# Kernel optimization log

Hardware: AMD Instinct MI355X
Metric: run time of the kernel (lower is better)

## Reference

```python
import jax, jax.numpy as jnp
import numpy as np

# config (from UnifiedAttentionConfig defaults)
D = 512; H = 8; C = 64; DQ = 256; NI = 2; CI = 64
TOPK = 32; LMAX = 16; NWIN = 128; ROPE_BASE = 10000.0
B = 1; T = 1024; LP = 8; P = T // LP
NEG = -1e30


def _rope_cache(seq_len, dim):
    half = dim // 2
    inv = 1.0 / (ROPE_BASE ** (jnp.arange(half, dtype=jnp.float32) / half))
    f = jnp.arange(seq_len, dtype=jnp.float32)[:, None] * inv[None, :]
    emb = jnp.concatenate([f, f], axis=-1)
    return jnp.cos(emb), jnp.sin(emb)


def _rot(x, cos, sin):
    half = x.shape[-1] // 2
    x1, x2 = x[..., :half], x[..., half:]
    return x * cos + jnp.concatenate([-x2, x1], axis=-1) * sin


def _rms(x, w, eps=1e-6):
    return x * jax.lax.rsqrt(jnp.mean(x * x, axis=-1, keepdims=True) + eps) * w


def _forward(h, W_dq, W_uq, W_csa_kv, W_csa_z, B_csa, W_idx_kv, W_idx_z, B_idx,
             W_iuq, W_w, W_swkv, qnorm_w, knorm_w, W_o, sink_logits,
             phrase_mask, phrase_token_idx, phrase_end_pos):
    Bq, Tq, Dq = h.shape
    Pn, Lmax = phrase_mask.shape[1], phrase_mask.shape[2]
    scale = 1.0 / jnp.sqrt(jnp.float32(C))
    cos, sin = _rope_cache(Tq, C)
    cos_i, sin_i = _rope_cache(Tq, CI)
    # ---- queries: compress -> up-project -> RMSNorm -> RoPE (per-token) ----
    q_lat = h @ W_dq                                      # (B,T,DQ)
    q = (q_lat @ W_uq).reshape(Bq, Tq, H, C)
    q = _rot(_rms(q, qnorm_w), cos[:, None, :], sin[:, None, :])
    # ---- gather phrase tokens ----
    idx = phrase_token_idx.reshape(Bq, Pn * Lmax)
    hp = jnp.take_along_axis(h, idx[:, :, None], axis=1).reshape(Bq, Pn, Lmax, Dq)
    m = phrase_mask                                       # (B,P,Lmax) bool
    # ---- multi-head phrase compression (CSA KV) ----
    c_tok = (hp @ W_csa_kv).reshape(Bq, Pn, Lmax, H, C)
    z = (hp @ W_csa_z).reshape(Bq, Pn, Lmax, H, C) + B_csa[None, None]
    z = jnp.where(m[..., None, None], z, NEG)
    g = jax.nn.softmax(z, axis=2)
    g = jnp.where(m.any(axis=2)[:, :, None, None, None], g, 0.0)
    c_csa = jnp.sum(g * c_tok, axis=2)                    # (B,P,H,C) values
    pos = jnp.clip(phrase_end_pos, 0, Tq - 1)
    k_csa = _rot(_rms(c_csa, knorm_w), cos[pos][:, :, None, :], sin[pos][:, :, None, :])
    # ---- single-head phrase compression (indexer keys) ----
    ck = hp @ W_idx_kv                                    # (B,P,Lmax,CI)
    zk = hp @ W_idx_z + B_idx[None, None]
    zk = jnp.where(m[..., None], zk, NEG)
    gk = jax.nn.softmax(zk, axis=2)
    gk = jnp.where(m.any(axis=2)[:, :, None, None], gk, 0.0)
    k_idx = jnp.sum(gk * ck, axis=2)                      # (B,P,CI)
    k_idx = _rot(k_idx, cos_i[pos], sin_i[pos])
    # ---- lightning indexer + causal top-k routing ----
    q_i = (q_lat @ W_iuq).reshape(Bq, Tq, NI, CI)
    s = jax.nn.relu(jnp.einsum('bthd,bpd->bthp', q_i, k_idx))
    I = jnp.sum(s * (h @ W_w)[..., None], axis=2)         # (B,T,P)
    t_idx = jnp.arange(Tq)
    valid = (phrase_end_pos[:, None, :] <= t_idx[None, :, None]) & (phrase_end_pos[:, None, :] >= 0)
    I = jnp.where(valid, I, NEG)
    vals, sel = jax.lax.top_k(I, TOPK)                    # (B,T,K)
    sel_ok = vals > NEG * 0.5
    k_sel = jnp.take_along_axis(k_csa[:, None], sel[:, :, :, None, None], axis=2)  # (B,T,K,H,C)
    v_sel = jnp.take_along_axis(c_csa[:, None], sel[:, :, :, None, None], axis=2)
    logit_csa = jnp.einsum('bthc,btkhc->bthk', q, k_sel) * scale
    logit_csa = jnp.where(sel_ok[:, :, None, :], logit_csa, NEG)
    # ---- sliding window (fixed mode) ----
    kv = (h @ W_swkv).reshape(Bq, Tq, H, C)
    k_sw = _rot(_rms(kv, knorm_w), cos[:, None, :], sin[:, None, :])
    widx = t_idx[:, None] + jnp.arange(NWIN)[None, :] - (NWIN - 1)  # (T,W)
    w_ok = widx >= 0
    widx_c = jnp.clip(widx, 0, Tq - 1)
    k_win = k_sw[:, widx_c]                               # (B,T,W,H,C)
    v_win = kv[:, widx_c]
    logit_sw = jnp.einsum('bthc,btwhc->bthw', q, k_win) * scale
    logit_sw = jnp.where(w_ok[None, :, None, :], logit_sw, NEG)
    # ---- single softmax over [csa | window | sink] ----
    sink = jnp.broadcast_to(sink_logits.reshape(1, 1, H, 1), (Bq, Tq, H, 1))
    pattn = jax.nn.softmax(jnp.concatenate([logit_csa, logit_sw, sink], axis=-1), axis=-1)
    out = jnp.einsum('bthk,btkhc->bthc', pattn[..., :TOPK], v_sel) \
        + jnp.einsum('bthw,btwhc->bthc', pattn[..., TOPK:TOPK + NWIN], v_win)
    return out.reshape(Bq, Tq, H * C) @ W_o


def setup_inputs() -> dict:
    key = jax.random.key(0)
    ks = jax.random.split(key, 16)
    nrm = lambda k, shp: 0.02 * jax.random.normal(k, shp, dtype=jnp.float32)
    # structured phrases: phrase p covers tokens [p*LP, p*LP+LP), padded to LMAX
    l = np.arange(LMAX)
    mask = np.broadcast_to(l < LP, (B, P, LMAX)).copy()
    tok = np.minimum(l, LP - 1)[None, :] + (np.arange(P) * LP)[:, None]
    tok = np.broadcast_to(tok, (B, P, LMAX)).copy()
    end = np.broadcast_to(np.arange(P) * LP + LP - 1, (B, P)).copy()
    pid = np.broadcast_to(np.arange(T) // LP, (B, T)).copy()
    return {
        'h': jax.random.normal(ks[0], (B, T, D), dtype=jnp.float32),
        'phrase_mask': jnp.asarray(mask, dtype=bool),
        'phrase_token_idx': jnp.asarray(tok, dtype=jnp.int32),
        'phrase_end_pos': jnp.asarray(end, dtype=jnp.int32),
        'phrase_id': jnp.asarray(pid, dtype=jnp.int32),
        'W_dq': nrm(ks[1], (D, DQ)),
        'W_uq': nrm(ks[2], (DQ, H * C)),
        'W_csa_kv': nrm(ks[3], (D, H * C)),
        'W_csa_z': nrm(ks[4], (D, H * C)),
        'B_csa': nrm(ks[5], (LMAX, H, C)),
        'W_idx_kv': nrm(ks[6], (D, CI)),
        'W_idx_z': nrm(ks[7], (D, CI)),
        'B_idx': nrm(ks[8], (LMAX, CI)),
        'W_iuq': nrm(ks[9], (DQ, NI * CI)),
        'W_w': nrm(ks[10], (D, NI)),
        'W_swkv': nrm(ks[11], (D, H * C)),
        'qnorm_w': jnp.ones((C,), dtype=jnp.float32),
        'knorm_w': jnp.ones((C,), dtype=jnp.float32),
        'W_o': nrm(ks[12], (H * C, D)),
        'sink_logits': nrm(ks[13], (H,)),
    }


def reference(h, phrase_mask, phrase_token_idx, phrase_end_pos, phrase_id,
              W_dq, W_uq, W_csa_kv, W_csa_z, B_csa, W_idx_kv, W_idx_z, B_idx,
              W_iuq, W_w, W_swkv, qnorm_w, knorm_w, W_o, sink_logits):
    del phrase_id  # only used when sw_mode == 'phrase'
    return _forward(h, W_dq, W_uq, W_csa_kv, W_csa_z, B_csa, W_idx_kv, W_idx_z,
                    B_idx, W_iuq, W_w, W_swkv, qnorm_w, knorm_w, W_o, sink_logits,
                    phrase_mask, phrase_token_idx, phrase_end_pos)
```

## Files before the change

kernel.cpp:

```cpp
#include <hip/hip_runtime.h>
#include <cmath>

static constexpr int Tn = 1024, Dn = 512, Hn = 8, Cn = 64, DQn = 256,
                     NIn = 2, CIn = 64, TK = 32, LM = 16, NW = 128, Pn = 128;
#define NEGV (-1e30f)

typedef unsigned short u16;
typedef __bf16 bf16x8 __attribute__((ext_vector_type(8)));
typedef float f32x4 __attribute__((ext_vector_type(4)));

__device__ __forceinline__ u16 f2bf(float x) {
  unsigned u = __float_as_uint(x);
  return (u16)((u + 0x7fffu + ((u >> 16) & 1u)) >> 16);
}
__device__ __forceinline__ float bf2f(u16 b) {
  return __uint_as_float((unsigned)b << 16);
}

struct PackJobs {
  const float* src[7];
  u16* dst[7];
  int start[8];
  int N[7];
  int logN[7];
  int isA[7];
  int ps[7];
};

__global__ __launch_bounds__(256) void pack_all(PackJobs pj) {
  int i = blockIdx.x * 256 + threadIdx.x;
  if (i >= pj.start[7]) return;
  int j = 0;
  while (i >= pj.start[j + 1]) ++j;
  int local = i - pj.start[j];
  const float* s = pj.src[j];
  u16* dh = pj.dst[j];
  u16* dl = dh + pj.ps[j];
  float x[8];
  size_t idx;
  if (pj.isA[j]) {
    int m = local & 1023;
    int kg = local >> 10;
    const float4* p = reinterpret_cast<const float4*>(s + (size_t)m * 512 + kg * 8);
    float4 a = p[0], b = p[1];
    x[0] = a.x; x[1] = a.y; x[2] = a.z; x[3] = a.w;
    x[4] = b.x; x[5] = b.y; x[6] = b.z; x[7] = b.w;
    idx = ((size_t)kg * 1024 + m) * 8;
  } else {
    int N = pj.N[j];
    int n = local & (N - 1);
    int kg = local >> pj.logN[j];
#pragma unroll
    for (int e = 0; e < 8; ++e) x[e] = s[(size_t)(kg * 8 + e) * N + n];
    idx = ((size_t)kg * N + n) * 8;
  }
  union { u16 u[8]; int4 v; } oh, ol;
#pragma unroll
  for (int e = 0; e < 8; ++e) {
    u16 hb = f2bf(x[e]);
    oh.u[e] = hb;
    ol.u[e] = f2bf(x[e] - bf2f(hb));
  }
  *reinterpret_cast<int4*>(dh + idx) = oh.v;
  *reinterpret_cast<int4*>(dl + idx) = ol.v;
}

struct TileDesc {
  const u16* Blo;
  const u16* Bhi;
  float* Clo;
  float* Chi;
  u16* Cp;
  int ldNlo, ldNhi, ldClo, ldChi, mode, n0, bps, cpps;
};
struct GemmArgs {
  TileDesc d[15];
};

#define GLD16(gp, lp)                                                     \
  __builtin_amdgcn_global_load_lds(                                      \
      (const __attribute__((address_space(1))) unsigned int*)(gp),       \
      (__attribute__((address_space(3))) unsigned int*)(lp), 16, 0, 0)

template <int FMW>
__global__ __launch_bounds__(256) void gemm_bf16(const u16* __restrict__ Ap,
                                                 int NK, int aps, GemmArgs ga) {
  constexpr int MT = FMW * 32;
  const int ct = blockIdx.x, rt = blockIdx.y;
  const TileDesc d = ga.d[ct];
  const int m0 = rt * MT;
  __shared__ __align__(16) u16 lA[2][2][4][MT][8];
  __shared__ __align__(16) u16 lB[2][2][4][128][8];
  const int tid = threadIdx.x;
  const int w = tid >> 6, lane = tid & 63;
  const int wm = w >> 1, wn = w & 1;

  f32x4 acc[FMW][4];
#pragma unroll
  for (int a = 0; a < FMW; ++a)
#pragma unroll
    for (int b = 0; b < 4; ++b)
#pragma unroll
      for (int r = 0; r < 4; ++r) acc[a][b][r] = 0.f;

  auto stage = [&](int buf, int kg) {
#pragma unroll
    for (int r0 = 0; r0 < MT; r0 += 64) {
      GLD16(Ap + ((size_t)kg * 1024 + m0 + r0 + lane) * 8, &lA[buf][0][w][r0][0]);
      GLD16(Ap + aps + ((size_t)kg * 1024 + m0 + r0 + lane) * 8, &lA[buf][1][w][r0][0]);
    }
    GLD16(d.Blo + ((size_t)kg * d.ldNlo + lane) * 8, &lB[buf][0][w][0][0]);
    GLD16(d.Bhi + ((size_t)kg * d.ldNhi + lane) * 8, &lB[buf][0][w][64][0]);
    GLD16(d.Blo + d.bps + ((size_t)kg * d.ldNlo + lane) * 8, &lB[buf][1][w][0][0]);
    GLD16(d.Bhi + d.bps + ((size_t)kg * d.ldNhi + lane) * 8, &lB[buf][1][w][64][0]);
  };

  stage(0, w);
  const int kq = lane >> 4, fr = lane & 15;
  for (int ks = 0; ks < NK; ++ks) {
    __syncthreads();
    if (ks + 1 < NK) stage((ks + 1) & 1, (ks + 1) * 4 + w);
    const int cb = ks & 1;
    bf16x8 aFh[FMW], aFl[FMW], bFh[4], bFl[4];
#pragma unroll
    for (int f = 0; f < FMW; ++f) {
      aFh[f] = *reinterpret_cast<const bf16x8*>(&lA[cb][0][kq][wm * (FMW * 16) + f * 16 + fr][0]);
      aFl[f] = *reinterpret_cast<const bf16x8*>(&lA[cb][1][kq][wm * (FMW * 16) + f * 16 + fr][0]);
    }
#pragma unroll
    for (int f = 0; f < 4; ++f) {
      bFh[f] = *reinterpret_cast<const bf16x8*>(&lB[cb][0][kq][wn * 64 + f * 16 + fr][0]);
      bFl[f] = *reinterpret_cast<const bf16x8*>(&lB[cb][1][kq][wn * 64 + f * 16 + fr][0]);
    }
#pragma unroll
    for (int fm = 0; fm < FMW; ++fm)
#pragma unroll
      for (int fn = 0; fn < 4; ++fn) {
        acc[fm][fn] = __builtin_amdgcn_mfma_f32_16x16x32_bf16(aFh[fm], bFh[fn],
                                                              acc[fm][fn], 0, 0, 0);
        acc[fm][fn] = __builtin_amdgcn_mfma_f32_16x16x32_bf16(aFl[fm], bFh[fn],
                                                              acc[fm][fn], 0, 0, 0);
        acc[fm][fn] = __builtin_amdgcn_mfma_f32_16x16x32_bf16(aFh[fm], bFl[fn],
                                                              acc[fm][fn], 0, 0, 0);
      }
  }
  float* Cb = (wn == 0) ? d.Clo : d.Chi;
  const int ldc = (wn == 0) ? d.ldClo : d.ldChi;
  if (d.mode != 1) {
#pragma unroll
    for (int fm = 0; fm < FMW; ++fm)
#pragma unroll
      for (int fn = 0; fn < 4; ++fn)
#pragma unroll
        for (int r = 0; r < 4; ++r) {
          int row = m0 + wm * (FMW * 16) + fm * 16 + (lane >> 4) * 4 + r;
          int cl = fn * 16 + fr;
          Cb[(size_t)row * ldc + cl] = acc[fm][fn][r];
        }
  }
  if (d.mode >= 1) {
#pragma unroll
    for (int fm = 0; fm < FMW; ++fm)
#pragma unroll
      for (int fn = 0; fn < 4; ++fn)
#pragma unroll
        for (int r = 0; r < 4; ++r) {
          int row = m0 + wm * (FMW * 16) + fm * 16 + (lane >> 4) * 4 + r;
          int gc = d.n0 + wn * 64 + fn * 16 + fr;
          float v = acc[fm][fn][r];
          u16 hb = f2bf(v);
          u16 lb = f2bf(v - bf2f(hb));
          size_t idx = ((size_t)(gc >> 3) * 1024 + row) * 8 + (gc & 7);
          d.Cp[idx] = hb;
          d.Cp[idx + d.cpps] = lb;
        }
  }
}

__global__ __launch_bounds__(256) void idx_kernel(
    const float* __restrict__ h, const float* __restrict__ q_lat,
    const float* __restrict__ Wikv, const float* __restrict__ Wiz,
    const float* __restrict__ Wiuq, float* __restrict__ hikv,
    float* __restrict__ hiz, float* __restrict__ qib) {
  const int t0 = blockIdx.x * 4;
  const int tid = threadIdx.x;
  __shared__ float hs[4][Dn];
  __shared__ float ql[4][DQn];
  for (int i = tid; i < 4 * Dn; i += 256)
    hs[i >> 9][i & 511] = h[(size_t)(t0 + (i >> 9)) * Dn + (i & 511)];
  for (int i = tid; i < 4 * DQn; i += 256)
    ql[i >> 8][i & 255] = q_lat[(size_t)(t0 + (i >> 8)) * DQn + (i & 255)];
  __syncthreads();
  if (tid < 128) {
    const float* Wm = (tid < 64) ? Wikv : Wiz;
    const int ci = tid & 63;
    float a0 = 0.f, a1 = 0.f, a2 = 0.f, a3 = 0.f;
#pragma unroll 8
    for (int k = 0; k < Dn; ++k) {
      float wv = Wm[k * CIn + ci];
      a0 += hs[0][k] * wv;
      a1 += hs[1][k] * wv;
      a2 += hs[2][k] * wv;
      a3 += hs[3][k] * wv;
    }
    float* dst = (tid < 64) ? hikv : hiz;
    dst[(size_t)(t0 + 0) * CIn + ci] = a0;
    dst[(size_t)(t0 + 1) * CIn + ci] = a1;
    dst[(size_t)(t0 + 2) * CIn + ci] = a2;
    dst[(size_t)(t0 + 3) * CIn + ci] = a3;
  } else {
    const int jj = tid - 128;
    float a0 = 0.f, a1 = 0.f, a2 = 0.f, a3 = 0.f;
#pragma unroll 8
    for (int k = 0; k < DQn; ++k) {
      float wv = Wiuq[k * 128 + jj];
      a0 += ql[0][k] * wv;
      a1 += ql[1][k] * wv;
      a2 += ql[2][k] * wv;
      a3 += ql[3][k] * wv;
    }
    qib[(size_t)(t0 + 0) * 128 + jj] = a0;
    qib[(size_t)(t0 + 1) * 128 + jj] = a1;
    qib[(size_t)(t0 + 2) * 128 + jj] = a2;
    qib[(size_t)(t0 + 3) * 128 + jj] = a3;
  }
}

__global__ __launch_bounds__(512) void phrase_rope_kernel(
    const int* __restrict__ maskbuf, const int* __restrict__ tokbuf,
    const int* __restrict__ endbuf, const float* __restrict__ hckv,
    const float* __restrict__ hcz, const float* __restrict__ hikv,
    const float* __restrict__ hiz, const float* __restrict__ Bcsa,
    const float* __restrict__ Bidx, const float* __restrict__ knw,
    const float* __restrict__ qnw, float* __restrict__ ccsa,
    float* __restrict__ kcsa, float* __restrict__ kidx,
    float* __restrict__ q, const float* __restrict__ kv,
    float* __restrict__ ksw) {
  const int tid = threadIdx.x;
  const int c = tid & 63;
  const float sgn = (c < 32) ? -1.f : 1.f;

  if (blockIdx.x >= Pn) {
    const int t = blockIdx.x - Pn;
    const float fr = (float)t * powf(10000.0f, -(float)(c & 31) / 32.0f);
    const float cv = cosf(fr), sv = sinf(fr);
    {
      float x = q[t * Dn + tid];
      float ss = x * x;
#pragma unroll
      for (int off = 32; off; off >>= 1) ss += __shfl_xor(ss, off, 64);
      float xr = x * rsqrtf(ss / (float)Cn + 1e-6f) * qnw[c];
      float pr = __shfl_xor(xr, 32, 64);
      q[t * Dn + tid] = xr * cv + sgn * pr * sv;
    }
    {
      float y = kv[t * Dn + tid];
      float ss = y * y;
#pragma unroll
      for (int off = 32; off; off >>= 1) ss += __shfl_xor(ss, off, 64);
      float yr = y * rsqrtf(ss / (float)Cn + 1e-6f) * knw[c];
      float pr = __shfl_xor(yr, 32, 64);
      ksw[t * Dn + tid] = yr * cv + sgn * pr * sv;
    }
    return;
  }

  const int p = blockIdx.x;
  __shared__ int s_bytemode;
  __shared__ int s_tok[LM];
  __shared__ int s_m[LM];
  __shared__ int s_pos, s_anyv;

  if (tid == 0) s_bytemode = 0;
  __syncthreads();
  {
    unsigned wv = ((const unsigned*)maskbuf)[tid];
    if (wv > 1u) atomicOr(&s_bytemode, 1);
  }
  __syncthreads();
  const int bytemode = s_bytemode;
  if (tid < LM) {
    int mv;
    if (bytemode)
      mv = ((const unsigned char*)maskbuf)[p * LM + tid] != 0;
    else
      mv = maskbuf[p * LM + tid] != 0;
    s_m[tid] = mv;
    s_tok[tid] = tokbuf[p * LM + tid];
  }
  if (tid == 0) {
    int e = endbuf[p];
    s_pos = min(max(e, 0), Tn - 1);
  }
  __syncthreads();
  if (tid == 0) {
    int any = 0;
    for (int l = 0; l < LM; ++l) any |= s_m[l];
    s_anyv = any;
  }
  __syncthreads();
  const int anyv = s_anyv;
  const int pos = s_pos;
  const float fr = (float)pos * powf(10000.0f, -(float)(c & 31) / 32.0f);
  const float cv = cosf(fr), sv = sinf(fr);

  {
    float z[LM];
    float zmax = NEGV;
#pragma unroll
    for (int l = 0; l < LM; ++l) {
      float zv = hcz[s_tok[l] * Dn + tid] + Bcsa[l * (Hn * Cn) + tid];
      zv = s_m[l] ? zv : NEGV;
      z[l] = zv;
      zmax = fmaxf(zmax, zv);
    }
    float den = 0.f, num = 0.f;
#pragma unroll
    for (int l = 0; l < LM; ++l) {
      float e = expf(z[l] - zmax);
      den += e;
      num += e * hckv[s_tok[l] * Dn + tid];
    }
    float cc = anyv ? (num / den) : 0.f;
    ccsa[p * (Hn * Cn) + tid] = cc;

    float ss = cc * cc;
#pragma unroll
    for (int off = 32; off; off >>= 1) ss += __shfl_xor(ss, off, 64);
    float kn = cc * rsqrtf(ss / (float)Cn + 1e-6f) * knw[c];
    float pr = __shfl_xor(kn, 32, 64);
    kcsa[p * (Hn * Cn) + tid] = kn * cv + sgn * pr * sv;
  }

  if (tid < CIn) {
    float zk[LM];
    float zm = NEGV;
#pragma unroll
    for (int l = 0; l < LM; ++l) {
      float zv = hiz[s_tok[l] * CIn + tid] + Bidx[l * CIn + tid];
      zv = s_m[l] ? zv : NEGV;
      zk[l] = zv;
      zm = fmaxf(zm, zv);
    }
    float dk = 0.f, nk = 0.f;
#pragma unroll
    for (int l = 0; l < LM; ++l) {
      float e = expf(zk[l] - zm);
      dk += e;
      nk += e * hikv[s_tok[l] * CIn + tid];
    }
    float ki = anyv ? (nk / dk) : 0.f;
    float pr = __shfl_xor(ki, 32, 64);
    kidx[p * CIn + tid] = ki * cv + sgn * pr * sv;
  }
}

__global__ __launch_bounds__(128) void score_topk_kernel(
    const float* __restrict__ hbuf, const float* __restrict__ Ww,
    const float* __restrict__ qi, const float* __restrict__ kidx,
    const int* __restrict__ endbuf, int* __restrict__ sel,
    int* __restrict__ selok) {
  const int t = blockIdx.x;
  const int tid = threadIdx.x;
  __shared__ float sqi[NIn * CIn];
  __shared__ float kT[CIn][Pn + 1];
  __shared__ float sI[Pn];
  __shared__ float sp0[128], sp1[128];

  sqi[tid] = qi[(size_t)t * (NIn * CIn) + tid];
#pragma unroll
  for (int it = 0; it < 16; ++it) {
    int idx4 = it * 128 + tid;
    float4 v = reinterpret_cast<const float4*>(kidx)[idx4];
    int p = idx4 >> 4;
    int c4 = (idx4 & 15) * 4;
    kT[c4 + 0][p] = v.x;
    kT[c4 + 1][p] = v.y;
    kT[c4 + 2][p] = v.z;
    kT[c4 + 3][p] = v.w;
  }
  float p0 = 0.f, p1 = 0.f;
#pragma unroll
  for (int e4 = 0; e4 < 4; ++e4) {
    int e = tid * 4 + e4;
    float hv = hbuf[(size_t)t * Dn + e];
    p0 += hv * Ww[e * NIn + 0];
    p1 += hv * Ww[e * NIn + 1];
  }
  sp0[tid] = p0;
  sp1[tid] = p1;
  __syncthreads();
  for (int srd = 64; srd; srd >>= 1) {
    if (tid < srd) {
      sp0[tid] += sp0[tid + srd];
      sp1[tid] += sp1[tid + srd];
    }
    __syncthreads();
  }
  const float ww0 = sp0[0], ww1 = sp1[0];

  {
    const int p = tid;
    float s0 = 0.f, s1 = 0.f;
#pragma unroll 16
    for (int ci = 0; ci < CIn; ++ci) {
      float kc = kT[ci][p];
      s0 += sqi[ci] * kc;
      s1 += sqi[CIn + ci] * kc;
    }
    float Iv = fmaxf(s0, 0.f) * ww0 + fmaxf(s1, 0.f) * ww1;
    int e = endbuf[p];
    if (!(e <= t && e >= 0)) Iv = NEGV;
    sI[p] = Iv;
  }
  __syncthreads();

  if (tid < 64) {
    float v0 = sI[tid], v1 = sI[tid + 64];
    for (int it = 0; it < TK; ++it) {
      float bv;
      int bi;
      if (v0 >= v1) { bv = v0; bi = tid; } else { bv = v1; bi = tid + 64; }
#pragma unroll
      for (int off = 32; off; off >>= 1) {
        float ov = __shfl_xor(bv, off, 64);
        int oi = __shfl_xor(bi, off, 64);
        if (ov > bv || (ov == bv && oi < bi)) { bv = ov; bi = oi; }
      }
      if (tid == 0) {
        sel[t * TK + it] = bi;
        selok[t * TK + it] = (bv > NEGV * 0.5f) ? 1 : 0;
      }
      if (bi == tid) v0 = -3.4e38f;
      if (bi == tid + 64) v1 = -3.4e38f;
    }
  }
}

__global__ __launch_bounds__(256) void attn4_kernel(
    const float* __restrict__ q, const float* __restrict__ ksw,
    const float* __restrict__ kv, const float* __restrict__ kcsa,
    const float* __restrict__ ccsa, const int* __restrict__ sel,
    const int* __restrict__ selok, const float* __restrict__ sink,
    u16* __restrict__ atp) {
  const int tid = threadIdx.x;
  const int wid = tid >> 6, lane = tid & 63;
  const int g = lane >> 4;
  const int gl = lane & 15;
  const int h = blockIdx.x >> 8;
  const int t = ((blockIdx.x & 255) << 2) + wid;

  __shared__ float slog[4][164];
  __shared__ int s_sel[4][TK];
  __shared__ int s_ok[4][TK];

  if (lane < TK) {
    s_sel[wid][lane] = sel[t * TK + lane];
    s_ok[wid][lane] = selok[t * TK + lane];
  }
  const int hc = h * Cn + gl * 4;
  const float4 qf = *reinterpret_cast<const float4*>(&q[t * Dn + hc]);
  float* myslog = slog[wid];

#pragma unroll 4
  for (int pass = 0; pass < 32; ++pass) {
    int w = pass * 4 + g;
    int src = t + w - (NW - 1);
    int srcc = max(src, 0);
    float4 kk = *reinterpret_cast<const float4*>(&ksw[srcc * Dn + hc]);
    float acc = qf.x * kk.x + qf.y * kk.y + qf.z * kk.z + qf.w * kk.w;
#pragma unroll
    for (int off = 1; off < 16; off <<= 1) acc += __shfl_xor(acc, off, 64);
    if (gl == 0) myslog[TK + w] = (src >= 0) ? acc * 0.125f : NEGV;
  }
#pragma unroll 2
  for (int pass = 0; pass < 8; ++pass) {
    int s = pass * 4 + g;
    int se = s_sel[wid][s];
    float4 kk = *reinterpret_cast<const float4*>(&kcsa[se * Dn + hc]);
    float acc = qf.x * kk.x + qf.y * kk.y + qf.z * kk.z + qf.w * kk.w;
#pragma unroll
    for (int off = 1; off < 16; off <<= 1) acc += __shfl_xor(acc, off, 64);
    if (gl == 0) myslog[s] = s_ok[wid][s] ? acc * 0.125f : NEGV;
  }
  if (lane == 0) myslog[160] = sink[h];

  float x0 = myslog[lane];
  float x1 = myslog[lane + 64];
  float x2 = (lane < 33) ? myslog[lane + 128] : NEGV;
  float m = fmaxf(x0, fmaxf(x1, x2));
#pragma unroll
  for (int off = 32; off; off >>= 1) m = fmaxf(m, __shfl_xor(m, off, 64));
  float e0 = expf(x0 - m), e1 = expf(x1 - m);
  float e2 = (lane < 33) ? expf(x2 - m) : 0.f;
  float sden = e0 + e1 + e2;
#pragma unroll
  for (int off = 32; off; off >>= 1) sden += __shfl_xor(sden, off, 64);
  const float inv = 1.f / sden;
  myslog[lane] = e0 * inv;
  myslog[lane + 64] = e1 * inv;
  if (lane < 33) myslog[lane + 128] = e2 * inv;

  float4 acc = make_float4(0.f, 0.f, 0.f, 0.f);
#pragma unroll 4
  for (int pass = 0; pass < 32; ++pass) {
    int w = pass * 4 + g;
    int src = t + w - (NW - 1);
    int srcc = max(src, 0);
    float pv = myslog[TK + w];
    pv = (src >= 0) ? pv : 0.f;
    float4 vv = *reinterpret_cast<const float4*>(&kv[srcc * Dn + hc]);
    acc.x += pv * vv.x;
    acc.y += pv * vv.y;
    acc.z += pv * vv.z;
    acc.w += pv * vv.w;
  }
#pragma unroll 2
  for (int pass = 0; pass < 8; ++pass) {
    int s = pass * 4 + g;
    float pv = myslog[s];
    int se = s_sel[wid][s];
    float4 vv = *reinterpret_cast<const float4*>(&ccsa[se * Dn + hc]);
    acc.x += pv * vv.x;
    acc.y += pv * vv.y;
    acc.z += pv * vv.z;
    acc.w += pv * vv.w;
  }
  acc.x += __shfl_xor(acc.x, 16, 64);
  acc.y += __shfl_xor(acc.y, 16, 64);
  acc.z += __shfl_xor(acc.z, 16, 64);
  acc.w += __shfl_xor(acc.w, 16, 64);
  acc.x += __shfl_xor(acc.x, 32, 64);
  acc.y += __shfl_xor(acc.y, 32, 64);
  acc.z += __shfl_xor(acc.z, 32, 64);
  acc.w += __shfl_xor(acc.w, 32, 64);
  if (lane < 16) {
    float vals[4] = {acc.x, acc.y, acc.z, acc.w};
    int colb = h * Cn + lane * 4;
#pragma unroll
    for (int r = 0; r < 4; ++r) {
      int gc = colb + r;
      float v = vals[r];
      u16 hb = f2bf(v);
      u16 lb = f2bf(v - bf2f(hb));
      size_t idx = ((size_t)(gc >> 3) * 1024 + t) * 8 + (gc & 7);
      atp[idx] = hb;
      atp[idx + 524288] = lb;
    }
  }
}

extern "C" void kernel_launch(void* const* d_in, const int* in_sizes, int n_in,
                              void* d_out, int out_size, void* d_ws,
                              size_t ws_size, hipStream_t stream) {
  const float* h = (const float*)d_in[0];
  const int* mask = (const int*)d_in[1];
  const int* tok = (const int*)d_in[2];
  const int* endp = (const int*)d_in[3];
  const float* W_dq = (const float*)d_in[5];
  const float* W_uq = (const float*)d_in[6];
  const float* W_csa_kv = (const float*)d_in[7];
  const float* W_csa_z = (const float*)d_in[8];
  const float* B_csa = (const float*)d_in[9];
  const float* W_idx_kv = (const float*)d_in[10];
  const float* W_idx_z = (const float*)d_in[11];
  const float* B_idx = (const float*)d_in[12];
  const float* W_iuq = (const float*)d_in[13];
  const float* W_w = (const float*)d_in[14];
  const float* W_swkv = (const float*)d_in[15];
  const float* qnw = (const float*)d_in[16];
  const float* knw = (const float*)d_in[17];
  const float* W_o = (const float*)d_in[18];
  const float* sink = (const float*)d_in[19];

  float* ws = (float*)d_ws;
  u16* hA = (u16*)(ws + 0);
  float* qbuf = ws + 0;
  u16* qlP = (u16*)(ws + 524288);
  float* hckv = ws + 786432;
  u16* atP = (u16*)(ws + 786432);
  float* hcz = ws + 1310720;
  float* kvb = ws + 1835008;
  float* hikv = ws + 2359296;
  float* hiz = ws + 2424832;
  float* q_lat = ws + 2490368;
  float* ccsa = ws + 2752512;
  float* kcsa = ws + 2818048;
  float* kidx = ws + 2883584;
  int* seli = (int*)(ws + 2891776);
  int* selok = (int*)(ws + 2924544);
  float* qib = ws + 2957312;
  float* kswb = ws + 3088384;
  u16* pW = (u16*)(ws + 3612672);
  u16* pWdq = pW;
  u16* pWckv = pW + 262144;
  u16* pWcz = pW + 786432;
  u16* pWsw = pW + 1310720;
  u16* pWuq = pW + 1835008;
  u16* pWo = pW + 2097152;
  float* outp = (float*)d_out;

  {
    PackJobs pj{};
    const float* srcs[7] = {h, W_dq, W_csa_kv, W_csa_z, W_swkv, W_uq, W_o};
    u16* dsts[7] = {hA, pWdq, pWckv, pWcz, pWsw, pWuq, pWo};
    int Ns[7] = {0, 256, 512, 512, 512, 512, 512};
    int logNs[7] = {0, 8, 9, 9, 9, 9, 9};
    int Ks[7] = {512, 512, 512, 512, 512, 256, 512};
    int isA[7] = {1, 0, 0, 0, 0, 0, 0};
    int pss[7] = {524288, 131072, 262144, 262144, 262144, 131072, 262144};
    int s = 0;
    for (int i = 0; i < 7; ++i) {
      pj.src[i] = srcs[i];
      pj.dst[i] = dsts[i];
      pj.N[i] = Ns[i];
      pj.logN[i] = logNs[i];
      pj.isA[i] = isA[i];
      pj.ps[i] = pss[i];
      pj.start[i] = s;
      s += isA[i] ? 1024 * (Ks[i] / 8) : (Ks[i] / 8) * Ns[i];
    }
    pj.start[7] = s;
    pack_all<<<(s + 255) / 256, 256, 0, stream>>>(pj);
  }

  auto normTile = [](const u16* pB, int N, int n0, float* C, int ldc, int bps) {
    TileDesc td{};
    td.Blo = pB + n0 * 8;
    td.Bhi = pB + (n0 + 64) * 8;
    td.ldNlo = td.ldNhi = N;
    td.Clo = C + n0;
    td.Chi = C + n0 + 64;
    td.ldClo = td.ldChi = ldc;
    td.mode = 0;
    td.bps = bps;
    return td;
  };

  {
    GemmArgs ga{};
    int nt = 0;
    for (int n0 = 0; n0 < 256; n0 += 128) {
      TileDesc td = normTile(pWdq, 256, n0, q_lat, 256, 131072);
      td.mode = 2;
      td.Cp = qlP;
      td.cpps = 262144;
      td.n0 = n0;
      ga.d[nt++] = td;
    }
    for (int n0 = 0; n0 < 512; n0 += 128) ga.d[nt++] = normTile(pWckv, 512, n0, hckv, 512, 262144);
    for (int n0 = 0; n0 < 512; n0 += 128) ga.d[nt++] = normTile(pWcz, 512, n0, hcz, 512, 262144);
    for (int n0 = 0; n0 < 512; n0 += 128) ga.d[nt++] = normTile(pWsw, 512, n0, kvb, 512, 262144);
    gemm_bf16<2><<<dim3(nt, 16), 256, 0, stream>>>(hA, 16, 524288, ga);
  }
  {
    GemmArgs ga{};
    int nt = 0;
    for (int n0 = 0; n0 < 512; n0 += 128) ga.d[nt++] = normTile(pWuq, 512, n0, qbuf, 512, 131072);
    gemm_bf16<2><<<dim3(nt, 16), 256, 0, stream>>>(qlP, 8, 262144, ga);
  }
  idx_kernel<<<Tn / 4, 256, 0, stream>>>(h, q_lat, W_idx_kv, W_idx_z, W_iuq,
                                         hikv, hiz, qib);
  phrase_rope_kernel<<<Pn + Tn, 512, 0, stream>>>(
      mask, tok, endp, hckv, hcz, hikv, hiz, B_csa, B_idx, knw, qnw, ccsa,
      kcsa, kidx, qbuf, kvb, kswb);
  score_topk_kernel<<<Tn, 128, 0, stream>>>(h, W_w, qib, kidx, endp, seli,
                                            selok);
  attn4_kernel<<<dim3(Tn / 4 * Hn), 256, 0, stream>>>(qbuf, kswb, kvb, kcsa,
                                                      ccsa, seli, selok, sink,
                                                      atP);
  {
    GemmArgs ga{};
    int nt = 0;
    for (int n0 = 0; n0 < 512; n0 += 128) ga.d[nt++] = normTile(pWo, 512, n0, outp, 512, 262144);
    gemm_bf16<2><<<dim3(nt, 16), 256, 0, stream>>>(atP, 16, 524288, ga);
  }
  (void)in_sizes; (void)n_in; (void)out_size; (void)ws_size;
}
```

Baseline: 136.6 us.

## Merge q up-projection GEMM with indexer kernel and widen attention blocks

```diff
diff --git a/kernel.cpp b/kernel.cpp
--- a/kernel.cpp
+++ b/kernel.cpp
@@ -177,19 +177,101 @@
   }
 }
 
-__global__ __launch_bounds__(256) void idx_kernel(
+struct GemmSh {
+  u16 lA[2][2][4][64][8];
+  u16 lB[2][2][4][128][8];
+};
+struct IdxSh {
+  float hs[4][Dn];
+  float ql[4][DQn];
+};
+
+__global__ __launch_bounds__(256) void k2idx_kernel(
+    const u16* __restrict__ Ap, int aps, GemmArgs ga,
     const float* __restrict__ h, const float* __restrict__ q_lat,
     const float* __restrict__ Wikv, const float* __restrict__ Wiz,
     const float* __restrict__ Wiuq, float* __restrict__ hikv,
     float* __restrict__ hiz, float* __restrict__ qib) {
-  const int t0 = blockIdx.x * 4;
+  __shared__ __align__(16) char smraw[sizeof(GemmSh)];
+  const int bid = blockIdx.x;
   const int tid = threadIdx.x;
-  __shared__ float hs[4][Dn];
-  __shared__ float ql[4][DQn];
+
+  if (bid < 64) {
+    GemmSh* sh = reinterpret_cast<GemmSh*>(smraw);
+    const int ct = bid & 3, rt = bid >> 2;
+    const TileDesc d = ga.d[ct];
+    const int m0 = rt * 64;
+    const int w = tid >> 6, lane = tid & 63;
+    const int wm = w >> 1, wn = w & 1;
+    constexpr int NK = 8;
+
+    f32x4 acc[2][4];
+#pragma unroll
+    for (int a = 0; a < 2; ++a)
+#pragma unroll
+      for (int b = 0; b < 4; ++b)
+#pragma unroll
+        for (int r = 0; r < 4; ++r) acc[a][b][r] = 0.f;
+
+    auto stage = [&](int buf, int kg) {
+      GLD16(Ap + ((size_t)kg * 1024 + m0 + lane) * 8, &sh->lA[buf][0][w][0][0]);
+      GLD16(Ap + aps + ((size_t)kg * 1024 + m0 + lane) * 8, &sh->lA[buf][1][w][0][0]);
+      GLD16(d.Blo + ((size_t)kg * d.ldNlo + lane) * 8, &sh->lB[buf][0][w][0][0]);
+      GLD16(d.Bhi + ((size_t)kg * d.ldNhi + lane) * 8, &sh->lB[buf][0][w][64][0]);
+      GLD16(d.Blo + d.bps + ((size_t)kg * d.ldNlo + lane) * 8, &sh->lB[buf][1][w][0][0]);
+      GLD16(d.Bhi + d.bps + ((size_t)kg * d.ldNhi + lane) * 8, &sh->lB[buf][1][w][64][0]);
+    };
+
+    stage(0, w);
+    const int kq = lane >> 4, fr = lane & 15;
+    for (int ks = 0; ks < NK; ++ks) {
+      __syncthreads();
+      if (ks + 1 < NK) stage((ks + 1) & 1, (ks + 1) * 4 + w);
+      const int cb = ks & 1;
+      bf16x8 aFh[2], aFl[2], bFh[4], bFl[4];
+#pragma unroll
+      for (int f = 0; f < 2; ++f) {
+        aFh[f] = *reinterpret_cast<const bf16x8*>(&sh->lA[cb][0][kq][wm * 32 + f * 16 + fr][0]);
+        aFl[f] = *reinterpret_cast<const bf16x8*>(&sh->lA[cb][1][kq][wm * 32 + f * 16 + fr][0]);
+      }
+#pragma unroll
+      for (int f = 0; f < 4; ++f) {
+        bFh[f] = *reinterpret_cast<const bf16x8*>(&sh->lB[cb][0][kq][wn * 64 + f * 16 + fr][0]);
+        bFl[f] = *reinterpret_cast<const bf16x8*>(&sh->lB[cb][1][kq][wn * 64 + f * 16 + fr][0]);
+      }
+#pragma unroll
+      for (int fm = 0; fm < 2; ++fm)
+#pragma unroll
+        for (int fn = 0; fn < 4; ++fn) {
+          acc[fm][fn] = __builtin_amdgcn_mfma_f32_16x16x32_bf16(aFh[fm], bFh[fn],
+                                                                acc[fm][fn], 0, 0, 0);
+          acc[fm][fn] = __builtin_amdgcn_mfma_f32_16x16x32_bf16(aFl[fm], bFh[fn],
+                                                                acc[fm][fn], 0, 0, 0);
+          acc[fm][fn] = __builtin_amdgcn_mfma_f32_16x16x32_bf16(aFh[fm], bFl[fn],
+                                                                acc[fm][fn], 0, 0, 0);
+        }
+    }
+    float* Cb = (wn == 0) ? d.Clo : d.Chi;
+    const int ldc = (wn == 0) ? d.ldClo : d.ldChi;
+#pragma unroll
+    for (int fm = 0; fm < 2; ++fm)
+#pragma unroll
+      for (int fn = 0; fn < 4; ++fn)
+#pragma unroll
+        for (int r = 0; r < 4; ++r) {
+          int row = m0 + wm * 32 + fm * 16 + (lane >> 4) * 4 + r;
+          int cl = fn * 16 + fr;
+          Cb[(size_t)row * ldc + cl] = acc[fm][fn][r];
+        }
+    return;
+  }
+
+  IdxSh* sh = reinterpret_cast<IdxSh*>(smraw);
+  const int t0 = (bid - 64) * 4;
   for (int i = tid; i < 4 * Dn; i += 256)
-    hs[i >> 9][i & 511] = h[(size_t)(t0 + (i >> 9)) * Dn + (i & 511)];
+    sh->hs[i >> 9][i & 511] = h[(size_t)(t0 + (i >> 9)) * Dn + (i & 511)];
   for (int i = tid; i < 4 * DQn; i += 256)
-    ql[i >> 8][i & 255] = q_lat[(size_t)(t0 + (i >> 8)) * DQn + (i & 255)];
+    sh->ql[i >> 8][i & 255] = q_lat[(size_t)(t0 + (i >> 8)) * DQn + (i & 255)];
   __syncthreads();
   if (tid < 128) {
     const float* Wm = (tid < 64) ? Wikv : Wiz;
@@ -198,10 +280,10 @@
 #pragma unroll 8
     for (int k = 0; k < Dn; ++k) {
       float wv = Wm[k * CIn + ci];
-      a0 += hs[0][k] * wv;
-      a1 += hs[1][k] * wv;
-      a2 += hs[2][k] * wv;
-      a3 += hs[3][k] * wv;
+      a0 += sh->hs[0][k] * wv;
+      a1 += sh->hs[1][k] * wv;
+      a2 += sh->hs[2][k] * wv;
+      a3 += sh->hs[3][k] * wv;
     }
     float* dst = (tid < 64) ? hikv : hiz;
     dst[(size_t)(t0 + 0) * CIn + ci] = a0;
@@ -214,10 +296,10 @@
 #pragma unroll 8
     for (int k = 0; k < DQn; ++k) {
       float wv = Wiuq[k * 128 + jj];
-      a0 += ql[0][k] * wv;
-      a1 += ql[1][k] * wv;
-      a2 += ql[2][k] * wv;
-      a3 += ql[3][k] * wv;
+      a0 += sh->ql[0][k] * wv;
+      a1 += sh->ql[1][k] * wv;
+      a2 += sh->ql[2][k] * wv;
+      a3 += sh->ql[3][k] * wv;
     }
     qib[(size_t)(t0 + 0) * 128 + jj] = a0;
     qib[(size_t)(t0 + 1) * 128 + jj] = a1;
@@ -437,7 +519,7 @@
   }
 }
 
-__global__ __launch_bounds__(256) void attn4_kernel(
+__global__ __launch_bounds__(512) void attn8_kernel(
     const float* __restrict__ q, const float* __restrict__ ksw,
     const float* __restrict__ kv, const float* __restrict__ kcsa,
     const float* __restrict__ ccsa, const int* __restrict__ sel,
@@ -447,12 +529,12 @@
   const int wid = tid >> 6, lane = tid & 63;
   const int g = lane >> 4;
   const int gl = lane & 15;
-  const int h = blockIdx.x >> 8;
-  const int t = ((blockIdx.x & 255) << 2) + wid;
-
-  __shared__ float slog[4][164];
-  __shared__ int s_sel[4][TK];
-  __shared__ int s_ok[4][TK];
+  const int h = blockIdx.x >> 7;
+  const int t = ((blockIdx.x & 127) << 3) + wid;
+
+  __shared__ float slog[8][164];
+  __shared__ int s_sel[8][TK];
+  __shared__ int s_ok[8][TK];
 
   if (lane < TK) {
     s_sel[wid][lane] = sel[t * TK + lane];
@@ -657,16 +739,16 @@
     GemmArgs ga{};
     int nt = 0;
     for (int n0 = 0; n0 < 512; n0 += 128) ga.d[nt++] = normTile(pWuq, 512, n0, qbuf, 512, 131072);
-    gemm_bf16<2><<<dim3(nt, 16), 256, 0, stream>>>(qlP, 8, 262144, ga);
-  }
-  idx_kernel<<<Tn / 4, 256, 0, stream>>>(h, q_lat, W_idx_kv, W_idx_z, W_iuq,
-                                         hikv, hiz, qib);
+    k2idx_kernel<<<64 + Tn / 4, 256, 0, stream>>>(qlP, 262144, ga, h, q_lat,
+                                                  W_idx_kv, W_idx_z, W_iuq,
+                                                  hikv, hiz, qib);
+  }
   phrase_rope_kernel<<<Pn + Tn, 512, 0, stream>>>(
       mask, tok, endp, hckv, hcz, hikv, hiz, B_csa, B_idx, knw, qnw, ccsa,
       kcsa, kidx, qbuf, kvb, kswb);
   score_topk_kernel<<<Tn, 128, 0, stream>>>(h, W_w, qib, kidx, endp, seli,
                                             selok);
-  attn4_kernel<<<dim3(Tn / 4 * Hn), 256, 0, stream>>>(qbuf, kswb, kvb, kcsa,
+  attn8_kernel<<<dim3(Tn / 8 * Hn), 512, 0, stream>>>(qbuf, kswb, kvb, kcsa,
                                                       ccsa, seli, selok, sink,
                                                       atP);
   {
```

Result: faster. 126.8 us, median of 2 (-7.1%).
